# Kernel optimization log

Measured on AMD Instinct MI355X. Metric: run time of the kernel, lower is better.

The kernel has to match this reference:

```python
import jax, jax.numpy as jnp
import numpy as np


def setup_inputs() -> dict:
    key = jax.random.key(0)
    ks = jax.random.split(key, 8)
    N, Z, H, B = 2_000_000, 32, 64, 1024
    z_local = jax.random.normal(ks[0], (N, Z), dtype=jnp.float32)
    batch_vec = jnp.sort(jax.random.randint(ks[1], (N,), 0, B))
    # gate_nn: Linear(z_dim, 1)
    Wg = jax.random.normal(ks[2], (Z, 1), dtype=jnp.float32) / np.sqrt(Z)
    bg = jnp.zeros((1,), dtype=jnp.float32)
    # film: Linear(z_dim, 64) -> ReLU -> Linear(64, 2*z_dim)
    W1 = jax.random.normal(ks[3], (Z, H), dtype=jnp.float32) / np.sqrt(Z)
    b1 = jnp.zeros((H,), dtype=jnp.float32)
    W2 = jax.random.normal(ks[4], (H, 2 * Z), dtype=jnp.float32) / np.sqrt(H)
    b2 = jnp.zeros((2 * Z,), dtype=jnp.float32)
    return {"z_local": z_local, "Wg": Wg, "bg": bg, "W1": W1, "b1": b1,
            "W2": W2, "b2": b2, "batch_vec": batch_vec, "num_graphs": B}


def reference(z_local, Wg, bg, W1, b1, W2, b2, batch_vec, num_graphs):
    # --- GlobalAttention: scatter-softmax over per-graph node segments ---
    gate = (z_local @ Wg + bg)[:, 0]                                   # [N]
    seg_max = jax.ops.segment_max(gate, batch_vec, num_segments=num_graphs)  # [B]
    e = jnp.exp(gate - seg_max[batch_vec])                              # [N], stable
    denom = jax.ops.segment_sum(e, batch_vec, num_segments=num_graphs)  # [B]
    alpha = e / denom[batch_vec]                                        # [N]
    g = jax.ops.segment_sum(alpha[:, None] * z_local, batch_vec,
                            num_segments=num_graphs)                    # [B, Z]
    g = jnp.where(denom[:, None] > 0, g, 0.0)  # guard empty segments
    # --- FiLM MLP: gamma/beta per graph ---
    h = jax.nn.relu(g @ W1 + b1)                                        # [B, 64]
    gb = h @ W2 + b2                                                    # [B, 2Z]
    Z = z_local.shape[1]
    gamma, beta = gb[:, :Z], gb[:, Z:]
    # broadcast per-graph FiLM params back to nodes
    z_mod = z_local * (1.0 + gamma[batch_vec]) + beta[batch_vec]        # [N, Z]
    return z_mod, g
```

## Files before the change

kernel.cpp:

```cpp
#include <hip/hip_runtime.h>

#define ZDIM 32
#define HDIM 64
#define BGRAPH 1024
#define CAP 2030
#define NTHREADS 1024

typedef float f4 __attribute__((ext_vector_type(4)));
typedef unsigned short u16x4 __attribute__((ext_vector_type(4)));

__device__ __forceinline__ unsigned short f2bf(float f) {
    unsigned int u = __float_as_uint(f);
    return (unsigned short)((u + 0x7FFFu + ((u >> 16) & 1u)) >> 16);
}
__device__ __forceinline__ float bf2f(unsigned short h) {
    return __uint_as_float(((unsigned int)h) << 16);
}

__global__ __launch_bounds__(256) void k_bounds(
    const int* __restrict__ bvec, int* __restrict__ bounds, int N)
{
    const long i = (long)blockIdx.x * 256 + threadIdx.x;
    if (i >= N) return;
    const int cur = bvec[i];
    if (i == 0) {
        for (int b = 0; b <= cur; ++b) bounds[b] = 0;
    } else {
        const int prev = bvec[i - 1];
        for (int b = prev + 1; b <= cur; ++b) bounds[b] = (int)i;
    }
    if (i == N - 1) {
        for (int b = cur + 1; b <= BGRAPH; ++b) bounds[b] = N;
    }
}

__global__ __launch_bounds__(NTHREADS) void k_fused(
    const float* __restrict__ z, const int* __restrict__ bounds,
    const float* __restrict__ Wg, const float* __restrict__ bgp,
    const float* __restrict__ W1, const float* __restrict__ b1,
    const float* __restrict__ W2, const float* __restrict__ b2,
    float* __restrict__ out, float* __restrict__ g_out)
{
    extern __shared__ u16x4 z16s[];
    __shared__ float accum[1 + ZDIM];
    __shared__ float gsh[ZDIM];
    __shared__ float hsh[HDIM];
    __shared__ __align__(16) float fbsh[2 * ZDIM];

    const int b    = blockIdx.x;
    const int tid  = threadIdx.x;
    const int lane = tid & 63;
    const int q    = tid & 7;

    if (tid < 1 + ZDIM) accum[tid] = 0.f;
    __syncthreads();

    const int  s     = bounds[b];
    const int  e_nd  = bounds[b + 1];
    const int  nf4   = (e_nd - s) * 8;
    const long base4 = (long)s * 8;

    const f4* z4  = (const f4*)z;
    const f4  wgq = ((const f4*)Wg)[q];
    const float bg0 = bgp[0];

    f4 acc; acc.x = acc.y = acc.z = acc.w = 0.f;
    float acc_e = 0.f;

#define GA_PROC(zz, kk)                                                     \
    {                                                                       \
        if ((kk) < CAP * 8) {                                               \
            u16x4 h;                                                        \
            h.x = f2bf((zz).x); h.y = f2bf((zz).y);                         \
            h.z = f2bf((zz).z); h.w = f2bf((zz).w);                         \
            z16s[kk] = h;                                                   \
        }                                                                   \
        float p = (zz).x * wgq.x + (zz).y * wgq.y +                         \
                  (zz).z * wgq.z + (zz).w * wgq.w;                          \
        p += __shfl_xor(p, 1);                                              \
        p += __shfl_xor(p, 2);                                              \
        p += __shfl_xor(p, 4);                                              \
        const float e = __expf(p + bg0);                                    \
        acc.x = fmaf(e, (zz).x, acc.x);                                     \
        acc.y = fmaf(e, (zz).y, acc.y);                                     \
        acc.z = fmaf(e, (zz).z, acc.z);                                     \
        acc.w = fmaf(e, (zz).w, acc.w);                                     \
        if (q == 0) acc_e += e;                                             \
    }

    int k = tid;
    for (; k + 3 * NTHREADS < nf4; k += 4 * NTHREADS) {
        const f4 a0 = z4[base4 + k];
        const f4 a1 = z4[base4 + k + 1 * NTHREADS];
        const f4 a2 = z4[base4 + k + 2 * NTHREADS];
        const f4 a3 = z4[base4 + k + 3 * NTHREADS];
        GA_PROC(a0, k);
        GA_PROC(a1, k + 1 * NTHREADS);
        GA_PROC(a2, k + 2 * NTHREADS);
        GA_PROC(a3, k + 3 * NTHREADS);
    }
    for (; k < nf4; k += NTHREADS) {
        const f4 a0 = z4[base4 + k];
        GA_PROC(a0, k);
    }
#undef GA_PROC

#pragma unroll
    for (int d = 8; d < 64; d <<= 1) {
        acc.x += __shfl_down(acc.x, d);
        acc.y += __shfl_down(acc.y, d);
        acc.z += __shfl_down(acc.z, d);
        acc.w += __shfl_down(acc.w, d);
        acc_e += __shfl_down(acc_e, d);
    }
    if (lane < 8) {
        atomicAdd(&accum[1 + q * 4 + 0], acc.x);
        atomicAdd(&accum[1 + q * 4 + 1], acc.y);
        atomicAdd(&accum[1 + q * 4 + 2], acc.z);
        atomicAdd(&accum[1 + q * 4 + 3], acc.w);
        if (lane == 0) atomicAdd(&accum[0], acc_e);
    }
    __syncthreads();

    if (tid < ZDIM) {
        const float dd = accum[0];
        const float gv = (dd > 0.f) ? accum[1 + tid] / dd : 0.f;
        gsh[tid] = gv;
        g_out[b * ZDIM + tid] = gv;
    }
    __syncthreads();
    if (tid < HDIM) {
        float hv = b1[tid];
#pragma unroll
        for (int kk = 0; kk < ZDIM; ++kk) hv = fmaf(gsh[kk], W1[kk * HDIM + tid], hv);
        hsh[tid] = fmaxf(hv, 0.f);
    }
    __syncthreads();
    if (tid < 2 * ZDIM) {
        float o = b2[tid];
#pragma unroll
        for (int h = 0; h < HDIM; ++h) o = fmaf(hsh[h], W2[h * (2 * ZDIM) + tid], o);
        fbsh[tid] = (tid < ZDIM) ? 1.0f + o : o;
    }
    __syncthreads();

    const f4 ga = ((const f4*)fbsh)[q];
    const f4 be = ((const f4*)fbsh)[8 + q];
    f4* out4 = (f4*)out;
    for (int kk = tid; kk < nf4; kk += NTHREADS) {
        f4 zz;
        if (kk < CAP * 8) {
            u16x4 h = z16s[kk];
            zz.x = bf2f(h.x); zz.y = bf2f(h.y); zz.z = bf2f(h.z); zz.w = bf2f(h.w);
        } else {
            zz = z4[base4 + kk];
        }
        f4 r;
        r.x = fmaf(zz.x, ga.x, be.x);
        r.y = fmaf(zz.y, ga.y, be.y);
        r.z = fmaf(zz.z, ga.z, be.z);
        r.w = fmaf(zz.w, ga.w, be.w);
        __builtin_nontemporal_store(r, &out4[base4 + kk]);
    }
}

extern "C" void kernel_launch(void* const* d_in, const int* in_sizes, int n_in,
                              void* d_out, int out_size, void* d_ws, size_t ws_size,
                              hipStream_t stream) {
    const float* z    = (const float*)d_in[0];
    const float* Wg   = (const float*)d_in[1];
    const float* bg   = (const float*)d_in[2];
    const float* W1   = (const float*)d_in[3];
    const float* b1   = (const float*)d_in[4];
    const float* W2   = (const float*)d_in[5];
    const float* b2   = (const float*)d_in[6];
    const int*   bvec = (const int*)d_in[7];
    const int N = in_sizes[7];

    int*   bounds = (int*)d_ws;
    float* out    = (float*)d_out;
    float* g_out  = out + (size_t)N * ZDIM;

    const int gridB = (N + 255) / 256;
    k_bounds<<<gridB, 256, 0, stream>>>(bvec, bounds, N);

    const size_t lds_bytes = (size_t)CAP * 8 * sizeof(u16x4);
    k_fused<<<BGRAPH, NTHREADS, lds_bytes, stream>>>(
        z, bounds, Wg, bg, W1, b1, W2, b2, out, g_out);
}
```

Measured before the change: 94.94 us.

## Process two graphs per block, overlapping next graph's gate pass with output pass

Each block now handles two consecutive graphs. The gate/softmax-accumulation pass for the second graph is interleaved with the FiLM output pass of the first graph, reusing the same LDS bf16 stash slot by slot. Then the second graph's MLP and output pass run. Grid size is halved. The aim is to overlap global reads with writes inside one block, since LDS use limits occupancy to one block per CU, and to cut serial phases per graph. The cost is added barriers, fewer blocks, and worse load balance if graph sizes vary.

After: 98.99 us. 1.04x slower.

```diff
diff --git a/kernel.cpp b/kernel.cpp
--- a/kernel.cpp
+++ b/kernel.cpp
@@ -47,7 +47,7 @@
     __shared__ float hsh[HDIM];
     __shared__ __align__(16) float fbsh[2 * ZDIM];
 
-    const int b    = blockIdx.x;
+    const int pb   = blockIdx.x;
     const int tid  = threadIdx.x;
     const int lane = tid & 63;
     const int q    = tid & 7;
@@ -55,26 +55,20 @@
     if (tid < 1 + ZDIM) accum[tid] = 0.f;
     __syncthreads();
 
-    const int  s     = bounds[b];
-    const int  e_nd  = bounds[b + 1];
-    const int  nf4   = (e_nd - s) * 8;
-    const long base4 = (long)s * 8;
+    const int  s0 = bounds[2 * pb];
+    const int  s1 = bounds[2 * pb + 1];
+    const int  s2 = bounds[2 * pb + 2];
+    const int  nfA = (s1 - s0) * 8;
+    const int  nfB = (s2 - s1) * 8;
+    const long baseA = (long)s0 * 8;
+    const long baseB = (long)s1 * 8;
 
     const f4* z4  = (const f4*)z;
     const f4  wgq = ((const f4*)Wg)[q];
     const float bg0 = bgp[0];
 
-    f4 acc; acc.x = acc.y = acc.z = acc.w = 0.f;
-    float acc_e = 0.f;
-
 #define GA_PROC(zz, kk)                                                     \
     {                                                                       \
-        if ((kk) < CAP * 8) {                                               \
-            u16x4 h;                                                        \
-            h.x = f2bf((zz).x); h.y = f2bf((zz).y);                         \
-            h.z = f2bf((zz).z); h.w = f2bf((zz).w);                         \
-            z16s[kk] = h;                                                   \
-        }                                                                   \
         float p = (zz).x * wgq.x + (zz).y * wgq.y +                         \
                   (zz).z * wgq.z + (zz).w * wgq.w;                          \
         p += __shfl_xor(p, 1);                                              \
@@ -87,24 +81,34 @@
         acc.w = fmaf(e, (zz).w, acc.w);                                     \
         if (q == 0) acc_e += e;                                             \
     }
-
-    int k = tid;
-    for (; k + 3 * NTHREADS < nf4; k += 4 * NTHREADS) {
-        const f4 a0 = z4[base4 + k];
-        const f4 a1 = z4[base4 + k + 1 * NTHREADS];
-        const f4 a2 = z4[base4 + k + 2 * NTHREADS];
-        const f4 a3 = z4[base4 + k + 3 * NTHREADS];
-        GA_PROC(a0, k);
-        GA_PROC(a1, k + 1 * NTHREADS);
-        GA_PROC(a2, k + 2 * NTHREADS);
-        GA_PROC(a3, k + 3 * NTHREADS);
-    }
-    for (; k < nf4; k += NTHREADS) {
-        const f4 a0 = z4[base4 + k];
-        GA_PROC(a0, k);
-    }
-#undef GA_PROC
-
+#define GA_STASH(zz, kk)                                                    \
+    if ((kk) < CAP * 8) {                                                   \
+        u16x4 h;                                                            \
+        h.x = f2bf((zz).x); h.y = f2bf((zz).y);                             \
+        h.z = f2bf((zz).z); h.w = f2bf((zz).w);                             \
+        z16s[kk] = h;                                                       \
+    }
+
+    f4 acc; acc.x = acc.y = acc.z = acc.w = 0.f;
+    float acc_e = 0.f;
+    {
+        int k = tid;
+        for (; k + 3 * NTHREADS < nfA; k += 4 * NTHREADS) {
+            const f4 a0 = z4[baseA + k];
+            const f4 a1 = z4[baseA + k + 1 * NTHREADS];
+            const f4 a2 = z4[baseA + k + 2 * NTHREADS];
+            const f4 a3 = z4[baseA + k + 3 * NTHREADS];
+            GA_STASH(a0, k);                    GA_PROC(a0, k);
+            GA_STASH(a1, k + 1 * NTHREADS);     GA_PROC(a1, k + 1 * NTHREADS);
+            GA_STASH(a2, k + 2 * NTHREADS);     GA_PROC(a2, k + 2 * NTHREADS);
+            GA_STASH(a3, k + 3 * NTHREADS);     GA_PROC(a3, k + 3 * NTHREADS);
+        }
+        for (; k < nfA; k += NTHREADS) {
+            const f4 a0 = z4[baseA + k];
+            GA_STASH(a0, k);
+            GA_PROC(a0, k);
+        }
+    }
 #pragma unroll
     for (int d = 8; d < 64; d <<= 1) {
         acc.x += __shfl_down(acc.x, d);
@@ -126,7 +130,7 @@
         const float dd = accum[0];
         const float gv = (dd > 0.f) ? accum[1 + tid] / dd : 0.f;
         gsh[tid] = gv;
-        g_out[b * ZDIM + tid] = gv;
+        g_out[2 * pb * ZDIM + tid] = gv;
     }
     __syncthreads();
     if (tid < HDIM) {
@@ -134,6 +138,8 @@
 #pragma unroll
         for (int kk = 0; kk < ZDIM; ++kk) hv = fmaf(gsh[kk], W1[kk * HDIM + tid], hv);
         hsh[tid] = fmaxf(hv, 0.f);
+    } else if (tid >= HDIM && tid < HDIM + 1 + ZDIM) {
+        accum[tid - HDIM] = 0.f;
     }
     __syncthreads();
     if (tid < 2 * ZDIM) {
@@ -144,24 +150,99 @@
     }
     __syncthreads();
 
-    const f4 ga = ((const f4*)fbsh)[q];
-    const f4 be = ((const f4*)fbsh)[8 + q];
+    const f4 gaA = ((const f4*)fbsh)[q];
+    const f4 beA = ((const f4*)fbsh)[8 + q];
     f4* out4 = (f4*)out;
-    for (int kk = tid; kk < nf4; kk += NTHREADS) {
+
+    acc.x = acc.y = acc.z = acc.w = 0.f;
+    acc_e = 0.f;
+    {
+        const int kmax = (nfA > nfB) ? nfA : nfB;
+        for (int k = tid; k < kmax; k += NTHREADS) {
+            f4 zb;
+            const bool vb = (k < nfB);
+            if (vb) zb = z4[baseB + k];
+            if (k < nfA) {
+                f4 za;
+                if (k < CAP * 8) {
+                    u16x4 h = z16s[k];
+                    za.x = bf2f(h.x); za.y = bf2f(h.y);
+                    za.z = bf2f(h.z); za.w = bf2f(h.w);
+                } else {
+                    za = z4[baseA + k];
+                }
+                f4 r;
+                r.x = fmaf(za.x, gaA.x, beA.x);
+                r.y = fmaf(za.y, gaA.y, beA.y);
+                r.z = fmaf(za.z, gaA.z, beA.z);
+                r.w = fmaf(za.w, gaA.w, beA.w);
+                __builtin_nontemporal_store(r, &out4[baseA + k]);
+            }
+            if (vb) {
+                GA_STASH(zb, k);
+                GA_PROC(zb, k);
+            }
+        }
+    }
+#pragma unroll
+    for (int d = 8; d < 64; d <<= 1) {
+        acc.x += __shfl_down(acc.x, d);
+        acc.y += __shfl_down(acc.y, d);
+        acc.z += __shfl_down(acc.z, d);
+        acc.w += __shfl_down(acc.w, d);
+        acc_e += __shfl_down(acc_e, d);
+    }
+    __syncthreads();
+    if (lane < 8) {
+        atomicAdd(&accum[1 + q * 4 + 0], acc.x);
+        atomicAdd(&accum[1 + q * 4 + 1], acc.y);
+        atomicAdd(&accum[1 + q * 4 + 2], acc.z);
+        atomicAdd(&accum[1 + q * 4 + 3], acc.w);
+        if (lane == 0) atomicAdd(&accum[0], acc_e);
+    }
+    __syncthreads();
+
+    if (tid < ZDIM) {
+        const float dd = accum[0];
+        const float gv = (dd > 0.f) ? accum[1 + tid] / dd : 0.f;
+        gsh[tid] = gv;
+        g_out[(2 * pb + 1) * ZDIM + tid] = gv;
+    }
+    __syncthreads();
+    if (tid < HDIM) {
+        float hv = b1[tid];
+#pragma unroll
+        for (int kk = 0; kk < ZDIM; ++kk) hv = fmaf(gsh[kk], W1[kk * HDIM + tid], hv);
+        hsh[tid] = fmaxf(hv, 0.f);
+    }
+    __syncthreads();
+    if (tid < 2 * ZDIM) {
+        float o = b2[tid];
+#pragma unroll
+        for (int h = 0; h < HDIM; ++h) o = fmaf(hsh[h], W2[h * (2 * ZDIM) + tid], o);
+        fbsh[tid] = (tid < ZDIM) ? 1.0f + o : o;
+    }
+    __syncthreads();
+
+    const f4 gaB = ((const f4*)fbsh)[q];
+    const f4 beB = ((const f4*)fbsh)[8 + q];
+    for (int k = tid; k < nfB; k += NTHREADS) {
         f4 zz;
-        if (kk < CAP * 8) {
-            u16x4 h = z16s[kk];
+        if (k < CAP * 8) {
+            u16x4 h = z16s[k];
             zz.x = bf2f(h.x); zz.y = bf2f(h.y); zz.z = bf2f(h.z); zz.w = bf2f(h.w);
         } else {
-            zz = z4[base4 + kk];
+            zz = z4[baseB + k];
         }
         f4 r;
-        r.x = fmaf(zz.x, ga.x, be.x);
-        r.y = fmaf(zz.y, ga.y, be.y);
-        r.z = fmaf(zz.z, ga.z, be.z);
-        r.w = fmaf(zz.w, ga.w, be.w);
-        __builtin_nontemporal_store(r, &out4[base4 + kk]);
-    }
+        r.x = fmaf(zz.x, gaB.x, beB.x);
+        r.y = fmaf(zz.y, gaB.y, beB.y);
+        r.z = fmaf(zz.z, gaB.z, beB.z);
+        r.w = fmaf(zz.w, gaB.w, beB.w);
+        __builtin_nontemporal_store(r, &out4[baseB + k]);
+    }
+#undef GA_PROC
+#undef GA_STASH
 }
 
 extern "C" void kernel_launch(void* const* d_in, const int* in_sizes, int n_in,
@@ -185,6 +266,6 @@
     k_bounds<<<gridB, 256, 0, stream>>>(bvec, bounds, N);
 
     const size_t lds_bytes = (size_t)CAP * 8 * sizeof(u16x4);
-    k_fused<<<BGRAPH, NTHREADS, lds_bytes, stream>>>(
+    k_fused<<<BGRAPH / 2, NTHREADS, lds_bytes, stream>>>(
         z, bounds, Wg, bg, W1, b1, W2, b2, out, g_out);
 }
```

## Process four graph segments per block in a persistent-style loop

Applied to the files above, without the earlier changes.

The fused kernel now launches a quarter as many blocks, and each block walks four consecutive graph segments in turn. The gate/softmax accumulation, the FiLM MLP and the output pass run once per segment, and the shared accumulators are reset between segments. This is meant to cut block launch and scheduling overhead, since the large LDS footprint already limits each CU to one block. In exchange, the dynamic load balancing across CUs is lost, so unevenly sized segments can leave some CUs idle longer at the tail.

New measurement: 166.1 us. 75.0% more time.

```diff
diff --git a/kernel.cpp b/kernel.cpp
--- a/kernel.cpp
+++ b/kernel.cpp
@@ -5,6 +5,7 @@
 #define BGRAPH 1024
 #define CAP 2030
 #define NTHREADS 1024
+#define SEGS 4
 
 typedef float f4 __attribute__((ext_vector_type(4)));
 typedef unsigned short u16x4 __attribute__((ext_vector_type(4)));
@@ -47,7 +48,6 @@
     __shared__ float hsh[HDIM];
     __shared__ __align__(16) float fbsh[2 * ZDIM];
 
-    const int b    = blockIdx.x;
     const int tid  = threadIdx.x;
     const int lane = tid & 63;
     const int q    = tid & 7;
@@ -55,26 +55,13 @@
     if (tid < 1 + ZDIM) accum[tid] = 0.f;
     __syncthreads();
 
-    const int  s     = bounds[b];
-    const int  e_nd  = bounds[b + 1];
-    const int  nf4   = (e_nd - s) * 8;
-    const long base4 = (long)s * 8;
-
     const f4* z4  = (const f4*)z;
     const f4  wgq = ((const f4*)Wg)[q];
     const float bg0 = bgp[0];
-
-    f4 acc; acc.x = acc.y = acc.z = acc.w = 0.f;
-    float acc_e = 0.f;
+    f4* out4 = (f4*)out;
 
 #define GA_PROC(zz, kk)                                                     \
     {                                                                       \
-        if ((kk) < CAP * 8) {                                               \
-            u16x4 h;                                                        \
-            h.x = f2bf((zz).x); h.y = f2bf((zz).y);                         \
-            h.z = f2bf((zz).z); h.w = f2bf((zz).w);                         \
-            z16s[kk] = h;                                                   \
-        }                                                                   \
         float p = (zz).x * wgq.x + (zz).y * wgq.y +                         \
                   (zz).z * wgq.z + (zz).w * wgq.w;                          \
         p += __shfl_xor(p, 1);                                              \
@@ -87,81 +74,103 @@
         acc.w = fmaf(e, (zz).w, acc.w);                                     \
         if (q == 0) acc_e += e;                                             \
     }
+#define GA_STASH(zz, kk)                                                    \
+    if ((kk) < CAP * 8) {                                                   \
+        u16x4 h;                                                            \
+        h.x = f2bf((zz).x); h.y = f2bf((zz).y);                             \
+        h.z = f2bf((zz).z); h.w = f2bf((zz).w);                             \
+        z16s[kk] = h;                                                       \
+    }
 
-    int k = tid;
-    for (; k + 3 * NTHREADS < nf4; k += 4 * NTHREADS) {
-        const f4 a0 = z4[base4 + k];
-        const f4 a1 = z4[base4 + k + 1 * NTHREADS];
-        const f4 a2 = z4[base4 + k + 2 * NTHREADS];
-        const f4 a3 = z4[base4 + k + 3 * NTHREADS];
-        GA_PROC(a0, k);
-        GA_PROC(a1, k + 1 * NTHREADS);
-        GA_PROC(a2, k + 2 * NTHREADS);
-        GA_PROC(a3, k + 3 * NTHREADS);
-    }
-    for (; k < nf4; k += NTHREADS) {
-        const f4 a0 = z4[base4 + k];
-        GA_PROC(a0, k);
+    for (int si = 0; si < SEGS; ++si) {
+        const int seg = blockIdx.x * SEGS + si;
+        const int s0  = bounds[seg];
+        const int s1  = bounds[seg + 1];
+        const int nf4 = (s1 - s0) * 8;
+        const long base4 = (long)s0 * 8;
+
+        f4 acc; acc.x = acc.y = acc.z = acc.w = 0.f;
+        float acc_e = 0.f;
+        {
+            int k = tid;
+            for (; k + 3 * NTHREADS < nf4; k += 4 * NTHREADS) {
+                const f4 a0 = z4[base4 + k];
+                const f4 a1 = z4[base4 + k + 1 * NTHREADS];
+                const f4 a2 = z4[base4 + k + 2 * NTHREADS];
+                const f4 a3 = z4[base4 + k + 3 * NTHREADS];
+                GA_STASH(a0, k);                GA_PROC(a0, k);
+                GA_STASH(a1, k + 1 * NTHREADS); GA_PROC(a1, k + 1 * NTHREADS);
+                GA_STASH(a2, k + 2 * NTHREADS); GA_PROC(a2, k + 2 * NTHREADS);
+                GA_STASH(a3, k + 3 * NTHREADS); GA_PROC(a3, k + 3 * NTHREADS);
+            }
+            for (; k < nf4; k += NTHREADS) {
+                const f4 a0 = z4[base4 + k];
+                GA_STASH(a0, k);
+                GA_PROC(a0, k);
+            }
+        }
+#pragma unroll
+        for (int d = 8; d < 64; d <<= 1) {
+            acc.x += __shfl_down(acc.x, d);
+            acc.y += __shfl_down(acc.y, d);
+            acc.z += __shfl_down(acc.z, d);
+            acc.w += __shfl_down(acc.w, d);
+            acc_e += __shfl_down(acc_e, d);
+        }
+        if (lane < 8) {
+            atomicAdd(&accum[1 + q * 4 + 0], acc.x);
+            atomicAdd(&accum[1 + q * 4 + 1], acc.y);
+            atomicAdd(&accum[1 + q * 4 + 2], acc.z);
+            atomicAdd(&accum[1 + q * 4 + 3], acc.w);
+            if (lane == 0) atomicAdd(&accum[0], acc_e);
+        }
+        __syncthreads();
+
+        if (tid < ZDIM) {
+            const float dd = accum[0];
+            const float gv = (dd > 0.f) ? accum[1 + tid] / dd : 0.f;
+            gsh[tid] = gv;
+            g_out[seg * ZDIM + tid] = gv;
+        }
+        __syncthreads();
+        if (tid < HDIM) {
+            float hv = b1[tid];
+#pragma unroll
+            for (int kk = 0; kk < ZDIM; ++kk) hv = fmaf(gsh[kk], W1[kk * HDIM + tid], hv);
+            hsh[tid] = fmaxf(hv, 0.f);
+        } else if (tid >= HDIM && tid < HDIM + 1 + ZDIM) {
+            accum[tid - HDIM] = 0.f;
+        }
+        __syncthreads();
+        if (tid < 2 * ZDIM) {
+            float o = b2[tid];
+#pragma unroll
+            for (int h = 0; h < HDIM; ++h) o = fmaf(hsh[h], W2[h * (2 * ZDIM) + tid], o);
+            fbsh[tid] = (tid < ZDIM) ? 1.0f + o : o;
+        }
+        __syncthreads();
+
+        const f4 ga = ((const f4*)fbsh)[q];
+        const f4 be = ((const f4*)fbsh)[8 + q];
+        for (int k = tid; k < nf4; k += NTHREADS) {
+            f4 zz;
+            if (k < CAP * 8) {
+                u16x4 h = z16s[k];
+                zz.x = bf2f(h.x); zz.y = bf2f(h.y);
+                zz.z = bf2f(h.z); zz.w = bf2f(h.w);
+            } else {
+                zz = z4[base4 + k];
+            }
+            f4 r;
+            r.x = fmaf(zz.x, ga.x, be.x);
+            r.y = fmaf(zz.y, ga.y, be.y);
+            r.z = fmaf(zz.z, ga.z, be.z);
+            r.w = fmaf(zz.w, ga.w, be.w);
+            __builtin_nontemporal_store(r, &out4[base4 + k]);
+        }
     }
 #undef GA_PROC
-
-#pragma unroll
-    for (int d = 8; d < 64; d <<= 1) {
-        acc.x += __shfl_down(acc.x, d);
-        acc.y += __shfl_down(acc.y, d);
-        acc.z += __shfl_down(acc.z, d);
-        acc.w += __shfl_down(acc.w, d);
-        acc_e += __shfl_down(acc_e, d);
-    }
-    if (lane < 8) {
-        atomicAdd(&accum[1 + q * 4 + 0], acc.x);
-        atomicAdd(&accum[1 + q * 4 + 1], acc.y);
-        atomicAdd(&accum[1 + q * 4 + 2], acc.z);
-        atomicAdd(&accum[1 + q * 4 + 3], acc.w);
-        if (lane == 0) atomicAdd(&accum[0], acc_e);
-    }
-    __syncthreads();
-
-    if (tid < ZDIM) {
-        const float dd = accum[0];
-        const float gv = (dd > 0.f) ? accum[1 + tid] / dd : 0.f;
-        gsh[tid] = gv;
-        g_out[b * ZDIM + tid] = gv;
-    }
-    __syncthreads();
-    if (tid < HDIM) {
-        float hv = b1[tid];
-#pragma unroll
-        for (int kk = 0; kk < ZDIM; ++kk) hv = fmaf(gsh[kk], W1[kk * HDIM + tid], hv);
-        hsh[tid] = fmaxf(hv, 0.f);
-    }
-    __syncthreads();
-    if (tid < 2 * ZDIM) {
-        float o = b2[tid];
-#pragma unroll
-        for (int h = 0; h < HDIM; ++h) o = fmaf(hsh[h], W2[h * (2 * ZDIM) + tid], o);
-        fbsh[tid] = (tid < ZDIM) ? 1.0f + o : o;
-    }
-    __syncthreads();
-
-    const f4 ga = ((const f4*)fbsh)[q];
-    const f4 be = ((const f4*)fbsh)[8 + q];
-    f4* out4 = (f4*)out;
-    for (int kk = tid; kk < nf4; kk += NTHREADS) {
-        f4 zz;
-        if (kk < CAP * 8) {
-            u16x4 h = z16s[kk];
-            zz.x = bf2f(h.x); zz.y = bf2f(h.y); zz.z = bf2f(h.z); zz.w = bf2f(h.w);
-        } else {
-            zz = z4[base4 + kk];
-        }
-        f4 r;
-        r.x = fmaf(zz.x, ga.x, be.x);
-        r.y = fmaf(zz.y, ga.y, be.y);
-        r.z = fmaf(zz.z, ga.z, be.z);
-        r.w = fmaf(zz.w, ga.w, be.w);
-        __builtin_nontemporal_store(r, &out4[base4 + kk]);
-    }
+#undef GA_STASH
 }
 
 extern "C" void kernel_launch(void* const* d_in, const int* in_sizes, int n_in,
@@ -185,6 +194,6 @@
     k_bounds<<<gridB, 256, 0, stream>>>(bvec, bounds, N);
 
     const size_t lds_bytes = (size_t)CAP * 8 * sizeof(u16x4);
-    k_fused<<<BGRAPH, NTHREADS, lds_bytes, stream>>>(
+    k_fused<<<BGRAPH / SEGS, NTHREADS, lds_bytes, stream>>>(
         z, bounds, Wg, bg, W1, b1, W2, b2, out, g_out);
 }
```
